# Kernel tuning notes

Hardware: AMD Instinct MI355X
Metric: run time of the kernel (lower is better)

Reference implementation:

```python
import jax, jax.numpy as jnp
import numpy as np

N = 8192
F_IN = 256
F_OUT = 128
SLOPE = 0.2
NEG_INF = -9000000000000000.0


def setup_inputs() -> dict:
    key = jax.random.key(0)
    k1, k2, k3, k4, k5 = jax.random.split(key, 5)
    x = jax.random.normal(k1, (N, F_IN), dtype=jnp.float32)
    adj = jax.random.randint(k2, (N, N), 0, 2).astype(jnp.float32)
    W = jax.random.normal(k3, (F_IN, F_OUT), dtype=jnp.float32) * (1.0 / np.sqrt(F_IN))
    a_src = jax.random.normal(k4, (F_OUT,), dtype=jnp.float32) * (1.0 / np.sqrt(F_OUT))
    a_dst = jax.random.normal(k5, (F_OUT,), dtype=jnp.float32) * (1.0 / np.sqrt(F_OUT))
    return {"x": x, "adj": adj, "W": W, "a_src": a_src, "a_dst": a_dst}


def reference(x, adj, W, a_src, a_dst):
    # h: (N, F_OUT)
    h = x @ W
    f_src = h @ a_src  # (N,)
    f_dst = h @ a_dst  # (N,)
    # additive attention scores: (N, N)
    e = f_src[:, None] + f_dst[None, :]
    e = jnp.where(e >= 0, e, SLOPE * e)  # leaky_relu
    e = jnp.where(adj > 0, e, NEG_INF)
    alpha = jax.nn.softmax(e, axis=1)  # (N, N)
    return alpha @ h  # (N, F_OUT)
```

## Files before the change

kernel.cpp:

```cpp
#include <hip/hip_runtime.h>
#include <hip/hip_bf16.h>

#define NN 8192
#define FIN 256
#define FO 128
#define ROWS 32
#define NCH 32
#define L2E 1.4426950408889634f
#define C2  0.28853900817779268f

typedef __bf16 bf16x8 __attribute__((ext_vector_type(8)));
typedef __bf16 bf16x2 __attribute__((ext_vector_type(2)));
typedef float  f32x4  __attribute__((ext_vector_type(4)));
typedef unsigned long long u64;
typedef u64 u64x2 __attribute__((ext_vector_type(2)));

__device__ __forceinline__ f32x4 ntload(const float* p) {
  return __builtin_nontemporal_load((const f32x4*)p);
}

__global__ __launch_bounds__(256) void k_proj(
    const float* __restrict__ x, const float* __restrict__ W,
    const float* __restrict__ a_src, const float* __restrict__ a_dst,
    __bf16* __restrict__ Bp, float* __restrict__ f_src, float* __restrict__ f_dst)
{
  __shared__ float xs[16 * FIN];
  __shared__ float fs[16], fd[16];
  const int tid = threadIdx.x;
  const int i0 = blockIdx.x * 16;

  const float4* xg = (const float4*)(x + (size_t)i0 * FIN);
  float4* xs4 = (float4*)xs;
  #pragma unroll
  for (int t = 0; t < 4; t++) xs4[tid + 256 * t] = xg[tid + 256 * t];
  if (tid < 16) { fs[tid] = 0.f; fd[tid] = 0.f; }
  __syncthreads();

  const int cq = tid & 31;
  const int rg = tid >> 5;
  const int c0 = cq * 4;
  const int r0 = rg * 2;
  float acc0[4] = {0.f,0.f,0.f,0.f};
  float acc1[4] = {0.f,0.f,0.f,0.f};
  const float* xr0 = xs + r0 * FIN;
  const float* xr1 = xs + (r0 + 1) * FIN;

  for (int k = 0; k < FIN; k += 4) {
    float4 xa = *(const float4*)(xr0 + k);
    float4 xb = *(const float4*)(xr1 + k);
    #pragma unroll
    for (int kk = 0; kk < 4; kk++) {
      float4 wv = *(const float4*)(W + (size_t)(k + kk) * FO + c0);
      float xav = ((const float*)&xa)[kk];
      float xbv = ((const float*)&xb)[kk];
      acc0[0] += xav * wv.x; acc0[1] += xav * wv.y;
      acc0[2] += xav * wv.z; acc0[3] += xav * wv.w;
      acc1[0] += xbv * wv.x; acc1[1] += xbv * wv.y;
      acc1[2] += xbv * wv.z; acc1[3] += xbv * wv.w;
    }
  }

  float4 as = *(const float4*)(a_src + c0);
  float4 ad = *(const float4*)(a_dst + c0);
  float ps0 = acc0[0]*as.x + acc0[1]*as.y + acc0[2]*as.z + acc0[3]*as.w;
  float ps1 = acc1[0]*as.x + acc1[1]*as.y + acc1[2]*as.z + acc1[3]*as.w;
  float pd0 = acc0[0]*ad.x + acc0[1]*ad.y + acc0[2]*ad.z + acc0[3]*ad.w;
  float pd1 = acc1[0]*ad.x + acc1[1]*ad.y + acc1[2]*ad.z + acc1[3]*ad.w;
  atomicAdd(&fs[r0],     ps0);
  atomicAdd(&fs[r0 + 1], ps1);
  atomicAdd(&fd[r0],     pd0);
  atomicAdd(&fd[r0 + 1], pd1);

  const int j0 = i0 + r0;
  const int kg = j0 >> 5;
  const int q  = (j0 >> 3) & 3;
  const int t0 = j0 & 7;
  #pragma unroll
  for (int c = 0; c < 4; c++) {
    const int n = c0 + c;
    bf16x2 v;
    v[0] = (__bf16)acc0[c];
    v[1] = (__bf16)acc1[c];
    size_t idx = ((size_t)(kg * 8 + (n >> 4)) * 64 + q * 16 + (n & 15)) * 8 + t0;
    *(bf16x2*)(Bp + idx) = v;
  }
  __syncthreads();
  if (tid < 16) { f_src[i0 + tid] = fs[tid]; f_dst[i0 + tid] = fd[tid]; }
}

__global__ __launch_bounds__(1024, 4) void k_attn(
    const float* __restrict__ adj, const __bf16* __restrict__ Bp,
    const float* __restrict__ f_src, const float* __restrict__ f_dst,
    float* __restrict__ out)
{
  __shared__ __align__(16) float G1[NN];
  __shared__ __align__(16) float G2[NN];
  __shared__ __align__(16) u64 msk[ROWS][6];
  __shared__ __align__(16) __bf16 af[2][8][64][8];
  __shared__ __align__(16) float ared[2][8][64][4];
  __shared__ float lsum[ROWS];

  const int tid = threadIdx.x;
  const int w = tid >> 6;
  const int lane = tid & 63;
  const int m = lane & 15;
  const int q = lane >> 4;
  const int i0 = blockIdx.x * ROWS;

  const int mtA = w >> 3;
  const int fA  = w & 7;
  const int sqA = fA >> 1, kgA = fA & 1;
  const int r0l = mtA * 16 + m;
  const int h   = w >> 3;
  const int nq8 = w & 7;

  const float* abase = adj + (size_t)(i0 + 2 * w) * NN + lane * 4;
  f32x4 sA0 = ntload(abase);
  f32x4 sA1 = ntload(abase + NN);
  f32x4 sB0 = ntload(abase + 256);
  f32x4 sB1 = ntload(abase + NN + 256);

  #pragma unroll
  for (int t = 0; t < NN / 1024; ++t) {
    int j = t * 1024 + tid;
    float d = f_dst[j];
    G1[j] = __builtin_amdgcn_exp2f(d * L2E);
    G2[j] = __builtin_amdgcn_exp2f(d * C2);
  }
  if (tid < ROWS) lsum[tid] = 0.f;
  float s = f_src[i0 + mtA * 16 + m];
  const float F1 = __builtin_amdgcn_exp2f(s * L2E);
  const float F2 = __builtin_amdgcn_exp2f(s * C2);

  f32x4 accP0 = (f32x4){0.f, 0.f, 0.f, 0.f};
  f32x4 accP1 = (f32x4){0.f, 0.f, 0.f, 0.f};
  float psum = 0.f;

#define ITER(c, s0, s1)                                                       \
  {                                                                           \
        \
    u64 b0 = __ballot(s0[0] > 0.f), b1 = __ballot(s0[1] > 0.f);               \
    u64 b2 = __ballot(s0[2] > 0.f), b3 = __ballot(s0[3] > 0.f);               \
    if (lane < 4) msk[2*w][lane]   = lane==0?b0:lane==1?b1:lane==2?b2:b3;     \
    b0 = __ballot(s1[0] > 0.f); b1 = __ballot(s1[1] > 0.f);                   \
    b2 = __ballot(s1[2] > 0.f); b3 = __ballot(s1[3] > 0.f);                   \
    if (lane < 4) msk[2*w+1][lane] = lane==0?b0:lane==1?b1:lane==2?b2:b3;     \
    __syncthreads();            \
                                    \
    {                                                                         \
      u64x2 Ma = *(const u64x2*)&msk[r0l][0];                                 \
      u64x2 Mb = *(const u64x2*)&msk[r0l][2];                                 \
      const u64 M0 = Ma[0], M1 = Ma[1], M2 = Mb[0], M3 = Mb[1];               \
      const int jj = (c) * 256 + sqA * 64 + kgA * 32 + q * 8;                 \
      float4 u0 = *(const float4*)(G1 + jj);                                  \
      float4 u1 = *(const float4*)(G1 + jj + 4);                              \
      float4 v0 = *(const float4*)(G2 + jj);                                  \
      float4 v1 = *(const float4*)(G2 + jj + 4);                              \
      const unsigned b = sqA * 16 + kgA * 8 + q * 2;                          \
      const unsigned e0 = (unsigned)(M0 >> b);                                \
      const unsigned e1 = (unsigned)(M1 >> b);                                \
      const unsigned e2 = (unsigned)(M2 >> b);                                \
      const unsigned e3 = (unsigned)(M3 >> b);                                \
      float p0 = (e0 & 1u) ? fmaxf(F1 * u0.x, F2 * v0.x) : 0.f;               \
      float p1 = (e1 & 1u) ? fmaxf(F1 * u0.y, F2 * v0.y) : 0.f;               \
      float p2 = (e2 & 1u) ? fmaxf(F1 * u0.z, F2 * v0.z) : 0.f;               \
      float p3 = (e3 & 1u) ? fmaxf(F1 * u0.w, F2 * v0.w) : 0.f;               \
      float p4 = (e0 & 2u) ? fmaxf(F1 * u1.x, F2 * v1.x) : 0.f;               \
      float p5 = (e1 & 2u) ? fmaxf(F1 * u1.y, F2 * v1.y) : 0.f;               \
      float p6 = (e2 & 2u) ? fmaxf(F1 * u1.z, F2 * v1.z) : 0.f;               \
      float p7 = (e3 & 2u) ? fmaxf(F1 * u1.w, F2 * v1.w) : 0.f;               \
      psum += ((p0 + p1) + (p2 + p3)) + ((p4 + p5) + (p6 + p7));              \
      bf16x8 a;                                                               \
      a[0] = (__bf16)p0; a[1] = (__bf16)p1; a[2] = (__bf16)p2;                \
      a[3] = (__bf16)p3; a[4] = (__bf16)p4; a[5] = (__bf16)p5;                \
      a[6] = (__bf16)p6; a[7] = (__bf16)p7;                                   \
      *(bf16x8*)&af[mtA][fA][lane][0] = a;                                    \
    }                                                                         \
    __syncthreads();                                   \
          \
    {                                                                         \
      const __bf16* bch = Bp + (size_t)((c) * 8 + h * 4) * 4096               \
                          + (size_t)nq8 * 512 + lane * 8;                     \
      bf16x8 bf0 = *(const bf16x8*)(bch);                                     \
      bf16x8 bf1 = *(const bf16x8*)(bch + 4096);                              \
      bf16x8 bf2 = *(const bf16x8*)(bch + 2 * 4096);                          \
      bf16x8 bf3 = *(const bf16x8*)(bch + 3 * 4096);                          \
      bf16x8 a00 = *(const bf16x8*)&af[0][h*4+0][lane][0];                    \
      bf16x8 a10 = *(const bf16x8*)&af[1][h*4+0][lane][0];                    \
      bf16x8 a01 = *(const bf16x8*)&af[0][h*4+1][lane][0];                    \
      bf16x8 a11 = *(const bf16x8*)&af[1][h*4+1][lane][0];                    \
      bf16x8 a02 = *(const bf16x8*)&af[0][h*4+2][lane][0];                    \
      bf16x8 a12 = *(const bf16x8*)&af[1][h*4+2][lane][0];                    \
      bf16x8 a03 = *(const bf16x8*)&af[0][h*4+3][lane][0];                    \
      bf16x8 a13 = *(const bf16x8*)&af[1][h*4+3][lane][0];                    \
      accP0 = __builtin_amdgcn_mfma_f32_16x16x32_bf16(a00, bf0, accP0, 0,0,0);\
      accP1 = __builtin_amdgcn_mfma_f32_16x16x32_bf16(a10, bf0, accP1, 0,0,0);\
      accP0 = __builtin_amdgcn_mfma_f32_16x16x32_bf16(a01, bf1, accP0, 0,0,0);\
      accP1 = __builtin_amdgcn_mfma_f32_16x16x32_bf16(a11, bf1, accP1, 0,0,0);\
      accP0 = __builtin_amdgcn_mfma_f32_16x16x32_bf16(a02, bf2, accP0, 0,0,0);\
      accP1 = __builtin_amdgcn_mfma_f32_16x16x32_bf16(a12, bf2, accP1, 0,0,0);\
      accP0 = __builtin_amdgcn_mfma_f32_16x16x32_bf16(a03, bf3, accP0, 0,0,0);\
      accP1 = __builtin_amdgcn_mfma_f32_16x16x32_bf16(a13, bf3, accP1, 0,0,0);\
    }                                                                         \
        \
    if ((c) + 2 < NCH) {                                                      \
      s0 = ntload(abase + ((c) + 2) * 256);                                   \
      s1 = ntload(abase + NN + ((c) + 2) * 256);                              \
    }                                                                         \
  }

  for (int c = 0; c < NCH; c += 2) {
    ITER(c, sA0, sA1)
    ITER(c + 1, sB0, sB1)
  }
#undef ITER

  {
    float p = psum;
    p += __shfl_xor(p, 16);
    p += __shfl_xor(p, 32);
    if (lane < 16) atomicAdd(&lsum[mtA * 16 + lane], p);
  }
  if (h == 0) {
    *(f32x4*)&ared[0][nq8][lane][0] = accP0;
    *(f32x4*)&ared[1][nq8][lane][0] = accP1;
  }
  __syncthreads();
  if (h == 1) {
    f32x4 r0v = *(const f32x4*)&ared[0][nq8][lane][0];
    f32x4 r1v = *(const f32x4*)&ared[1][nq8][lane][0];
    f32x4 o0 = accP0 + r0v;
    f32x4 o1 = accP1 + r1v;
    #pragma unroll
    for (int r = 0; r < 4; ++r) {
      const int rr = q * 4 + r;
      float inv0 = 1.0f / lsum[rr];
      float inv1 = 1.0f / lsum[16 + rr];
      out[(size_t)(i0 + rr) * FO + nq8 * 16 + m]      = o0[r] * inv0;
      out[(size_t)(i0 + 16 + rr) * FO + nq8 * 16 + m] = o1[r] * inv1;
    }
  }
}

extern "C" void kernel_launch(void* const* d_in, const int* in_sizes, int n_in,
                              void* d_out, int out_size, void* d_ws, size_t ws_size,
                              hipStream_t stream) {
  const float* x     = (const float*)d_in[0];
  const float* adj   = (const float*)d_in[1];
  const float* W     = (const float*)d_in[2];
  const float* a_src = (const float*)d_in[3];
  const float* a_dst = (const float*)d_in[4];
  float* out = (float*)d_out;

  char* ws = (char*)d_ws;
  __bf16* Bp   = (__bf16*)ws;
  float* f_src = (float*)(ws + 2097152);
  float* f_dst = (float*)(ws + 2097152 + 32768);

  hipLaunchKernelGGL(k_proj, dim3(512), dim3(256), 0, stream,
                     x, W, a_src, a_dst, Bp, f_src, f_dst);
  hipLaunchKernelGGL(k_attn, dim3(256), dim3(1024), 0, stream,
                     adj, Bp, f_src, f_dst, out);
}
```

Before: 395.1 us.

## Halve attention block to 16 rows and stream exp tables per chunk

The attention kernel now processes 16 rows per block with 512 threads (8 waves) instead of 32 rows with 1024 threads, and launches 512 blocks. Each wave owns one 16-column output slice and accumulates over the full K chunk, which removes the cross-half reduction through shared memory. The full 64 KB precomputed exp(f_dst) tables are replaced by double-buffered per-chunk 256-entry tables computed inside the loop, cutting LDS use so more blocks fit per CU. The cost is that every block reloads the Bp features for half as many rows, doubling total Bp traffic, and adds exp work inside the loop.

```diff
diff --git a/kernel.cpp b/kernel.cpp
--- a/kernel.cpp
+++ b/kernel.cpp
@@ -4,7 +4,7 @@
 #define NN 8192
 #define FIN 256
 #define FO 128
-#define ROWS 32
+#define BROWS 16
 #define NCH 32
 #define L2E 1.4426950408889634f
 #define C2  0.28853900817779268f
@@ -88,31 +88,27 @@
   if (tid < 16) { f_src[i0 + tid] = fs[tid]; f_dst[i0 + tid] = fd[tid]; }
 }
 
-__global__ __launch_bounds__(1024, 4) void k_attn(
+__global__ __launch_bounds__(512, 4) void k_attn(
     const float* __restrict__ adj, const __bf16* __restrict__ Bp,
     const float* __restrict__ f_src, const float* __restrict__ f_dst,
     float* __restrict__ out)
 {
-  __shared__ __align__(16) float G1[NN];
-  __shared__ __align__(16) float G2[NN];
-  __shared__ __align__(16) u64 msk[ROWS][6];
-  __shared__ __align__(16) __bf16 af[2][8][64][8];
-  __shared__ __align__(16) float ared[2][8][64][4];
-  __shared__ float lsum[ROWS];
+  __shared__ __align__(16) float G1s[2][256];
+  __shared__ __align__(16) float G2s[2][256];
+  __shared__ __align__(16) u64 msk[BROWS][6];
+  __shared__ __align__(16) __bf16 af[8][64][8];
+  __shared__ float lsum[BROWS];
 
   const int tid = threadIdx.x;
   const int w = tid >> 6;
   const int lane = tid & 63;
   const int m = lane & 15;
   const int q = lane >> 4;
-  const int i0 = blockIdx.x * ROWS;
-
-  const int mtA = w >> 3;
-  const int fA  = w & 7;
-  const int sqA = fA >> 1, kgA = fA & 1;
-  const int r0l = mtA * 16 + m;
-  const int h   = w >> 3;
-  const int nq8 = w & 7;
+  const int i0 = blockIdx.x * BROWS;
+
+  const int sqA = w >> 1, kgA = w & 1;
+  const int nq8 = w;
+  const int tbl = tid >> 8, gcol = tid & 255;
 
   const float* abase = adj + (size_t)(i0 + 2 * w) * NN + lane * 4;
   f32x4 sA0 = ntload(abase);
@@ -120,42 +116,44 @@
   f32x4 sB0 = ntload(abase + 256);
   f32x4 sB1 = ntload(abase + NN + 256);
 
-  #pragma unroll
-  for (int t = 0; t < NN / 1024; ++t) {
-    int j = t * 1024 + tid;
-    float d = f_dst[j];
-    G1[j] = __builtin_amdgcn_exp2f(d * L2E);
-    G2[j] = __builtin_amdgcn_exp2f(d * C2);
-  }
-  if (tid < ROWS) lsum[tid] = 0.f;
-  float s = f_src[i0 + mtA * 16 + m];
+  {
+    float d0 = f_dst[gcol];
+    if (tbl == 0) G1s[0][gcol] = __builtin_amdgcn_exp2f(d0 * L2E);
+    else          G2s[0][gcol] = __builtin_amdgcn_exp2f(d0 * C2);
+  }
+  float fdv = f_dst[256 + gcol];
+  if (tid < BROWS) lsum[tid] = 0.f;
+  float s = f_src[i0 + m];
   const float F1 = __builtin_amdgcn_exp2f(s * L2E);
   const float F2 = __builtin_amdgcn_exp2f(s * C2);
 
-  f32x4 accP0 = (f32x4){0.f, 0.f, 0.f, 0.f};
-  f32x4 accP1 = (f32x4){0.f, 0.f, 0.f, 0.f};
+  f32x4 acc = (f32x4){0.f, 0.f, 0.f, 0.f};
   float psum = 0.f;
 
 #define ITER(c, s0, s1)                                                       \
   {                                                                           \
-        \
+            \
     u64 b0 = __ballot(s0[0] > 0.f), b1 = __ballot(s0[1] > 0.f);               \
     u64 b2 = __ballot(s0[2] > 0.f), b3 = __ballot(s0[3] > 0.f);               \
     if (lane < 4) msk[2*w][lane]   = lane==0?b0:lane==1?b1:lane==2?b2:b3;     \
     b0 = __ballot(s1[0] > 0.f); b1 = __ballot(s1[1] > 0.f);                   \
     b2 = __ballot(s1[2] > 0.f); b3 = __ballot(s1[3] > 0.f);                   \
     if (lane < 4) msk[2*w+1][lane] = lane==0?b0:lane==1?b1:lane==2?b2:b3;     \
-    __syncthreads();            \
-                                    \
+    if ((c) + 1 < NCH) {                                                      \
+      if (tbl == 0) G1s[((c)+1)&1][gcol] = __builtin_amdgcn_exp2f(fdv * L2E); \
+      else          G2s[((c)+1)&1][gcol] = __builtin_amdgcn_exp2f(fdv * C2);  \
+    }                                                                         \
+    __syncthreads();                         \
+                \
     {                                                                         \
-      u64x2 Ma = *(const u64x2*)&msk[r0l][0];                                 \
-      u64x2 Mb = *(const u64x2*)&msk[r0l][2];                                 \
+      u64x2 Ma = *(const u64x2*)&msk[m][0];                                   \
+      u64x2 Mb = *(const u64x2*)&msk[m][2];                                   \
       const u64 M0 = Ma[0], M1 = Ma[1], M2 = Mb[0], M3 = Mb[1];               \
-      const int jj = (c) * 256 + sqA * 64 + kgA * 32 + q * 8;                 \
-      float4 u0 = *(const float4*)(G1 + jj);                                  \
-      float4 u1 = *(const float4*)(G1 + jj + 4);                              \
-      float4 v0 = *(const float4*)(G2 + jj);                                  \
-      float4 v1 = *(const float4*)(G2 + jj + 4);                              \
+      const int jl = sqA * 64 + kgA * 32 + q * 8;                             \
+      float4 u0 = *(const float4*)(&G1s[(c)&1][jl]);                          \
+      float4 u1 = *(const float4*)(&G1s[(c)&1][jl + 4]);                      \
+      float4 v0 = *(const float4*)(&G2s[(c)&1][jl]);                          \
+      float4 v1 = *(const float4*)(&G2s[(c)&1][jl + 4]);                      \
       const unsigned b = sqA * 16 + kgA * 8 + q * 2;                          \
       const unsigned e0 = (unsigned)(M0 >> b);                                \
       const unsigned e1 = (unsigned)(M1 >> b);                                \
@@ -174,38 +172,43 @@
       a[0] = (__bf16)p0; a[1] = (__bf16)p1; a[2] = (__bf16)p2;                \
       a[3] = (__bf16)p3; a[4] = (__bf16)p4; a[5] = (__bf16)p5;                \
       a[6] = (__bf16)p6; a[7] = (__bf16)p7;                                   \
-      *(bf16x8*)&af[mtA][fA][lane][0] = a;                                    \
+      *(bf16x8*)&af[w][lane][0] = a;                                          \
     }                                                                         \
     __syncthreads();                                   \
-          \
+                    \
     {                                                                         \
-      const __bf16* bch = Bp + (size_t)((c) * 8 + h * 4) * 4096               \
+      const __bf16* bch = Bp + (size_t)(c) * 8 * 4096                         \
                           + (size_t)nq8 * 512 + lane * 8;                     \
       bf16x8 bf0 = *(const bf16x8*)(bch);                                     \
       bf16x8 bf1 = *(const bf16x8*)(bch + 4096);                              \
       bf16x8 bf2 = *(const bf16x8*)(bch + 2 * 4096);                          \
       bf16x8 bf3 = *(const bf16x8*)(bch + 3 * 4096);                          \
-      bf16x8 a00 = *(const bf16x8*)&af[0][h*4+0][lane][0];                    \
-      bf16x8 a10 = *(const bf16x8*)&af[1][h*4+0][lane][0];                    \
-      bf16x8 a01 = *(const bf16x8*)&af[0][h*4+1][lane][0];                    \
-      bf16x8 a11 = *(const bf16x8*)&af[1][h*4+1][lane][0];                    \
-      bf16x8 a02 = *(const bf16x8*)&af[0][h*4+2][lane][0];                    \
-      bf16x8 a12 = *(const bf16x8*)&af[1][h*4+2][lane][0];                    \
-      bf16x8 a03 = *(const bf16x8*)&af[0][h*4+3][lane][0];                    \
-      bf16x8 a13 = *(const bf16x8*)&af[1][h*4+3][lane][0];                    \
-      accP0 = __builtin_amdgcn_mfma_f32_16x16x32_bf16(a00, bf0, accP0, 0,0,0);\
-      accP1 = __builtin_amdgcn_mfma_f32_16x16x32_bf16(a10, bf0, accP1, 0,0,0);\
-      accP0 = __builtin_amdgcn_mfma_f32_16x16x32_bf16(a01, bf1, accP0, 0,0,0);\
-      accP1 = __builtin_amdgcn_mfma_f32_16x16x32_bf16(a11, bf1, accP1, 0,0,0);\
-      accP0 = __builtin_amdgcn_mfma_f32_16x16x32_bf16(a02, bf2, accP0, 0,0,0);\
-      accP1 = __builtin_amdgcn_mfma_f32_16x16x32_bf16(a12, bf2, accP1, 0,0,0);\
-      accP0 = __builtin_amdgcn_mfma_f32_16x16x32_bf16(a03, bf3, accP0, 0,0,0);\
-      accP1 = __builtin_amdgcn_mfma_f32_16x16x32_bf16(a13, bf3, accP1, 0,0,0);\
-    }                                                                         \
-        \
+      bf16x8 bf4 = *(const bf16x8*)(bch + 4 * 4096);                          \
+      bf16x8 bf5 = *(const bf16x8*)(bch + 5 * 4096);                          \
+      bf16x8 bf6 = *(const bf16x8*)(bch + 6 * 4096);                          \
+      bf16x8 bf7 = *(const bf16x8*)(bch + 7 * 4096);                          \
+      bf16x8 a0 = *(const bf16x8*)&af[0][lane][0];                            \
+      bf16x8 a1 = *(const bf16x8*)&af[1][lane][0];                            \
+      bf16x8 a2 = *(const bf16x8*)&af[2][lane][0];                            \
+      bf16x8 a3 = *(const bf16x8*)&af[3][lane][0];                            \
+      bf16x8 a4 = *(const bf16x8*)&af[4][lane][0];                            \
+      bf16x8 a5 = *(const bf16x8*)&af[5][lane][0];                            \
+      bf16x8 a6 = *(const bf16x8*)&af[6][lane][0];                            \
+      bf16x8 a7 = *(const bf16x8*)&af[7][lane][0];                            \
+      acc = __builtin_amdgcn_mfma_f32_16x16x32_bf16(a0, bf0, acc, 0, 0, 0);   \
+      acc = __builtin_amdgcn_mfma_f32_16x16x32_bf16(a1, bf1, acc, 0, 0, 0);   \
+      acc = __builtin_amdgcn_mfma_f32_16x16x32_bf16(a2, bf2, acc, 0, 0, 0);   \
+      acc = __builtin_amdgcn_mfma_f32_16x16x32_bf16(a3, bf3, acc, 0, 0, 0);   \
+      acc = __builtin_amdgcn_mfma_f32_16x16x32_bf16(a4, bf4, acc, 0, 0, 0);   \
+      acc = __builtin_amdgcn_mfma_f32_16x16x32_bf16(a5, bf5, acc, 0, 0, 0);   \
+      acc = __builtin_amdgcn_mfma_f32_16x16x32_bf16(a6, bf6, acc, 0, 0, 0);   \
+      acc = __builtin_amdgcn_mfma_f32_16x16x32_bf16(a7, bf7, acc, 0, 0, 0);   \
+    }                                                                         \
+     \
     if ((c) + 2 < NCH) {                                                      \
       s0 = ntload(abase + ((c) + 2) * 256);                                   \
       s1 = ntload(abase + NN + ((c) + 2) * 256);                              \
+      fdv = f_dst[((c) + 2) * 256 + gcol];                                    \
     }                                                                         \
   }
 
@@ -219,26 +222,15 @@
     float p = psum;
     p += __shfl_xor(p, 16);
     p += __shfl_xor(p, 32);
-    if (lane < 16) atomicAdd(&lsum[mtA * 16 + lane], p);
-  }
-  if (h == 0) {
-    *(f32x4*)&ared[0][nq8][lane][0] = accP0;
-    *(f32x4*)&ared[1][nq8][lane][0] = accP1;
+    if (lane < 16) atomicAdd(&lsum[lane], p);
   }
   __syncthreads();
-  if (h == 1) {
-    f32x4 r0v = *(const f32x4*)&ared[0][nq8][lane][0];
-    f32x4 r1v = *(const f32x4*)&ared[1][nq8][lane][0];
-    f32x4 o0 = accP0 + r0v;
-    f32x4 o1 = accP1 + r1v;
-    #pragma unroll
-    for (int r = 0; r < 4; ++r) {
-      const int rr = q * 4 + r;
-      float inv0 = 1.0f / lsum[rr];
-      float inv1 = 1.0f / lsum[16 + rr];
-      out[(size_t)(i0 + rr) * FO + nq8 * 16 + m]      = o0[r] * inv0;
-      out[(size_t)(i0 + 16 + rr) * FO + nq8 * 16 + m] = o1[r] * inv1;
-    }
+
+  #pragma unroll
+  for (int r = 0; r < 4; ++r) {
+    const int rr = q * 4 + r;
+    const float inv = 1.0f / lsum[rr];
+    out[(size_t)(i0 + rr) * FO + nq8 * 16 + m] = acc[r] * inv;
   }
 }
 
@@ -259,6 +251,6 @@
 
   hipLaunchKernelGGL(k_proj, dim3(512), dim3(256), 0, stream,
                      x, W, a_src, a_dst, Bp, f_src, f_dst);
-  hipLaunchKernelGGL(k_attn, dim3(256), dim3(1024), 0, stream,
+  hipLaunchKernelGGL(k_attn, dim3(512), dim3(512), 0, stream,
                      adj, Bp, f_src, f_dst, out);
 }
```

New measurement: 406.6 us. 2.9% more time.
